# Performance work log

Measured on AMD Instinct MI355X. Metric: run time of the kernel, lower is better.

The kernel has to match this reference:

```python
import jax, jax.numpy as jnp
import numpy as np

B, N, D = 2, 4096, 256
H = 8
HD = D // H  # head dim = 32
DFF = 4 * D


def _layer_norm(x):
    # Matches source: (x - mean) / (std + 1e-6), std is population std (ddof=0)
    m = jnp.mean(x, axis=-1, keepdims=True)
    s = jnp.std(x, axis=-1, keepdims=True)
    return (x - m) / (s + 1e-6)


def setup_inputs() -> dict:
    key = jax.random.key(0)
    ks = jax.random.split(key, 11)
    sd = 1.0 / np.sqrt(D)
    sf = 1.0 / np.sqrt(DFF)
    return {
        "embeddings_in": jax.random.normal(ks[0], (B, N, D), dtype=jnp.float32),
        "Wq": jax.random.normal(ks[1], (D, D), dtype=jnp.float32) * sd,
        "bq": jnp.zeros((D,), dtype=jnp.float32),
        "Wk": jax.random.normal(ks[2], (D, D), dtype=jnp.float32) * sd,
        "bk": jnp.zeros((D,), dtype=jnp.float32),
        "Wv": jax.random.normal(ks[3], (D, D), dtype=jnp.float32) * sd,
        "bv": jnp.zeros((D,), dtype=jnp.float32),
        "Wo": jax.random.normal(ks[4], (D, D), dtype=jnp.float32) * sd,
        "bo": jnp.zeros((D,), dtype=jnp.float32),
        "W1": jax.random.normal(ks[5], (D, DFF), dtype=jnp.float32) * sd,
        "b1": jnp.zeros((DFF,), dtype=jnp.float32),
        "W2": jax.random.normal(ks[6], (DFF, D), dtype=jnp.float32) * sf,
        "b2": jnp.zeros((D,), dtype=jnp.float32),
    }


def reference(embeddings_in, Wq, bq, Wk, bk, Wv, bv, Wo, bo, W1, b1, W2, b2):
    x = embeddings_in
    xn1 = _layer_norm(x)
    # QKV projections, split into heads: [B,N,D] -> [B,H,N,HD]
    def heads(t):
        return jnp.transpose(t.reshape(B, N, H, HD), (0, 2, 1, 3))
    q = heads(xn1 @ Wq + bq)
    k = heads(xn1 @ Wk + bk)
    v = heads(xn1 @ Wv + bv)
    scores = jnp.einsum('bhnd,bhmd->bhnm', q, k) / jnp.sqrt(jnp.float32(HD))
    attn = jax.nn.softmax(scores, axis=-1)
    heads_out = jnp.einsum('bhnm,bhmd->bhnd', attn, v)
    attn_out = jnp.transpose(heads_out, (0, 2, 1, 3)).reshape(B, N, D)
    attn_out = attn_out @ Wo + bo  # dropout is identity in eval
    x_skip = attn_out + x
    xn2 = _layer_norm(x_skip)
    mlp = jax.nn.gelu(xn2 @ W1 + b1) @ W2 + b2
    return mlp + x_skip
```

## Files before the change

kernel.cpp:

```cpp
#include <hip/hip_runtime.h>
#include <hip/hip_bf16.h>

#define Bb 2
#define Nn 4096
#define Dd 256
#define Hh 8
#define HDh 32
#define DFFd 1024
#define MT (Bb*Nn)
#define Tt ((size_t)MT * Dd)
#define SPLIT 4
#define KVB (Nn / SPLIT)
#define NSTP (KVB / 64)

typedef __attribute__((ext_vector_type(8))) short short8;
typedef __attribute__((ext_vector_type(4))) float f32x4;
typedef __attribute__((address_space(1))) const unsigned int gu32;
typedef __attribute__((address_space(3))) unsigned int lu32;

__device__ __forceinline__ void gll16(const ushort* g, ushort* l) {
  __builtin_amdgcn_global_load_lds((gu32*)g, (lu32*)l, 16, 0, 0);
}
__device__ __forceinline__ float bf2f(ushort u){
  union { unsigned int i; float f; } v; v.i = ((unsigned int)u) << 16; return v.f;
}
__device__ __forceinline__ ushort f2bf(float f){
  union { float f; unsigned int i; } v; v.f = f;
  unsigned int r = v.i + 0x7fffu + ((v.i >> 16) & 1u);
  return (ushort)(r >> 16);
}
__device__ __forceinline__ int ars(int r){ return r * 64 + (r >> 3) * 32; }

__device__ __forceinline__ void ln_rows4(const float* __restrict__ x,
                                         ushort* __restrict__ out, int row0,
                                         int wave, int lane)
{
  #pragma unroll
  for (int r = 0; r < 4; r++) {
    const int row = row0 + wave * 4 + r;
    const float4 u = *(const float4*)(x + (size_t)row * Dd + lane * 4);
    float s1 = u.x + u.y + u.z + u.w;
    float s2 = u.x*u.x + u.y*u.y + u.z*u.z + u.w*u.w;
    #pragma unroll
    for (int m = 1; m < 64; m <<= 1) { s1 += __shfl_xor(s1, m, 64); s2 += __shfl_xor(s2, m, 64); }
    const float mean = s1 * (1.0f / Dd);
    float var = s2 * (1.0f / Dd) - mean * mean;
    var = var < 0.f ? 0.f : var;
    const float inv = 1.0f / (sqrtf(var) + 1e-6f);
    ushort4 o;
    o.x = f2bf((u.x - mean) * inv); o.y = f2bf((u.y - mean) * inv);
    o.z = f2bf((u.z - mean) * inv); o.w = f2bf((u.w - mean) * inv);
    *(ushort4*)(out + (size_t)row * Dd + lane * 4) = o;
  }
}

__global__ __launch_bounds__(256) void p0_kernel(
    const float* __restrict__ Wq, const float* __restrict__ Wk,
    const float* __restrict__ Wv, const float* __restrict__ Wo,
    const float* __restrict__ W1, const float* __restrict__ W2,
    const float* __restrict__ bq, const float* __restrict__ bk,
    const float* __restrict__ bv, ushort* __restrict__ wt,
    float* __restrict__ bqkv, const float* __restrict__ x,
    ushort* __restrict__ xn1)
{
  const int bid = blockIdx.x, t = threadIdx.x;
  __shared__ __align__(16) ushort T[64][72];
  if (bid < 192) {
    const float* src; ushort* dst; int Nsrc, Kdst, kt, nt;
    if (bid < 64) {
      const int m = bid >> 4, tile = bid & 15;
      kt = tile >> 2; nt = tile & 3; Nsrc = 256; Kdst = 256;
      src = (m == 0 ? Wq : m == 1 ? Wk : m == 2 ? Wv : Wo);
      dst = (m == 3) ? (wt + 196608) : (wt + m * 65536);
    } else if (bid < 128) {
      const int tile = bid - 64; kt = tile >> 4; nt = tile & 15;
      Nsrc = 1024; Kdst = 256; src = W1; dst = wt + 262144;
    } else {
      const int tile = bid - 128; kt = tile >> 2; nt = tile & 3;
      Nsrc = 256; Kdst = 1024; src = W2; dst = wt + 524288;
    }
    const int k0 = kt * 64, n0 = nt * 64;
    const int cc = t & 15, rr = t >> 4;
    #pragma unroll
    for (int pass = 0; pass < 4; pass++) {
      const int k = rr + pass * 16;
      const float4 v = *(const float4*)(src + (size_t)(k0 + k) * Nsrc + n0 + cc * 4);
      T[cc * 4 + 0][k] = f2bf(v.x); T[cc * 4 + 1][k] = f2bf(v.y);
      T[cc * 4 + 2][k] = f2bf(v.z); T[cc * 4 + 3][k] = f2bf(v.w);
    }
    __syncthreads();
    const int nl = t >> 2, ks = (t & 3) * 16;
    const short8 a = *(const short8*)(&T[nl][ks]);
    const short8 b = *(const short8*)(&T[nl][ks + 8]);
    ushort* drow = dst + (size_t)(n0 + nl) * Kdst + k0 + ks;
    *(short8*)(drow) = a; *(short8*)(drow + 8) = b;
  } else if (bid == 192) {
    bqkv[t] = bq[t]; bqkv[256 + t] = bk[t]; bqkv[512 + t] = bv[t];
  }
  ln_rows4(x, xn1, bid * 16, t >> 6, t & 63);
}

__global__ __launch_bounds__(256) void ln_kernel(const float* __restrict__ x,
                                                 ushort* __restrict__ out)
{
  ln_rows4(x, out, blockIdx.x * 16, threadIdx.x >> 6, threadIdx.x & 63);
}

template<int EPI>
__global__ __launch_bounds__(256) void gemm_wide(
    const ushort* __restrict__ A, const ushort* __restrict__ BT,
    const float* __restrict__ bias, void* __restrict__ outv, int N, int K)
{
  __shared__ __align__(16) ushort As[2][128 * 64];
  __shared__ __align__(16) ushort Bs[2][128 * 64];
  const int tid = threadIdx.x;
  const int wave = tid >> 6, lane = tid & 63;
  const int quad = lane >> 4, l15 = lane & 15;
  const int wm = wave >> 1, wn = wave & 1;
  const int n0 = blockIdx.x * 128, m0 = blockIdx.y * 128;
  f32x4 acc[4][4];
  #pragma unroll
  for (int mt = 0; mt < 4; mt++)
    #pragma unroll
    for (int nt = 0; nt < 4; nt++) acc[mt][nt] = (f32x4){0.f,0.f,0.f,0.f};
  const int srow = lane >> 3, scol = ((lane & 7) ^ srow) * 8;
  const ushort* gA[4];
  const ushort* gB[4];
  #pragma unroll
  for (int i = 0; i < 4; i++) {
    gA[i] = A  + (size_t)(m0 + i * 32 + wave * 8 + srow) * K + scol;
    gB[i] = BT + (size_t)(n0 + i * 32 + wave * 8 + srow) * K + scol;
  }
  int aoff[4], boff[4], cx[2];
  #pragma unroll
  for (int mt = 0; mt < 4; mt++) aoff[mt] = (wm * 64 + mt * 16 + l15) * 64;
  #pragma unroll
  for (int nt = 0; nt < 4; nt++) boff[nt] = (wn * 64 + nt * 16 + l15) * 64;
  #pragma unroll
  for (int kk = 0; kk < 2; kk++) cx[kk] = ((kk * 4 + quad) ^ (l15 & 7)) * 8;
  #pragma unroll
  for (int i = 0; i < 4; i++) {
    gll16(gA[i], &As[0][(i * 32 + wave * 8) * 64]);
    gll16(gB[i], &Bs[0][(i * 32 + wave * 8) * 64]);
  }
  __syncthreads();
  const int NC = K >> 6;
  int p = 0;
  for (int c = 0; c < NC; c++) {
    if (c + 1 < NC) {
      #pragma unroll
      for (int i = 0; i < 4; i++) {
        gll16(gA[i] + (c + 1) * 64, &As[p ^ 1][(i * 32 + wave * 8) * 64]);
        gll16(gB[i] + (c + 1) * 64, &Bs[p ^ 1][(i * 32 + wave * 8) * 64]);
      }
    }
    #pragma unroll
    for (int kk = 0; kk < 2; kk++) {
      short8 af[4];
      #pragma unroll
      for (int mt = 0; mt < 4; mt++)
        af[mt] = *(const short8*)(&As[p][aoff[mt] + cx[kk]]);
      #pragma unroll
      for (int nt = 0; nt < 4; nt++) {
        const short8 bf = *(const short8*)(&Bs[p][boff[nt] + cx[kk]]);
        #pragma unroll
        for (int mt = 0; mt < 4; mt++)
          acc[mt][nt] = __builtin_amdgcn_mfma_f32_16x16x32_bf16(af[mt], bf, acc[mt][nt], 0, 0, 0);
      }
    }
    __syncthreads();
    p ^= 1;
  }
  #pragma unroll
  for (int mt = 0; mt < 4; mt++) {
    const int row0 = m0 + wm * 64 + mt * 16 + quad * 4;
    #pragma unroll
    for (int nt = 0; nt < 4; nt++) {
      const int col = n0 + wn * 64 + nt * 16 + l15;
      const float bv = bias[col];
      float c[4];
      #pragma unroll
      for (int i = 0; i < 4; i++) c[i] = acc[mt][nt][i] + bv;
      if (EPI == 0) {
        ushort* qkv = (ushort*)outv;
        const int w = col >> 8, cd = col & 255;
        const int h = cd >> 5, hd = cd & 31;
        const int b = row0 >> 12, n = row0 & (Nn - 1);
        if (w < 2) {
          const float sc2 = (w == 0) ? (1.4426950408889634f * 0.17677669529663687f) : 1.0f;
          ushort* dst = qkv + (size_t)w * Tt + ((size_t)((b * Hh + h) * Nn) + n) * HDh + hd;
          #pragma unroll
          for (int i = 0; i < 4; i++) dst[(size_t)i * HDh] = f2bf(c[i] * sc2);
        } else {
          ushort4 pk;
          pk.x = f2bf(c[0]); pk.y = f2bf(c[1]); pk.z = f2bf(c[2]); pk.w = f2bf(c[3]);
          *(ushort4*)(qkv + 2 * Tt + ((size_t)((b * Hh + h) * HDh + hd)) * Nn + n) = pk;
        }
      } else {
        ushort* out = (ushort*)outv;
        #pragma unroll
        for (int i = 0; i < 4; i++) {
          const float t = tanhf(0.7978845608028654f * (c[i] + 0.044715f * c[i] * c[i] * c[i]));
          out[(size_t)(row0 + i) * N + col] = f2bf(0.5f * c[i] * (1.0f + t));
        }
      }
    }
  }
}

template<int EPI, int BM>
__global__ __launch_bounds__(256) void gemm_epi(
    const ushort* __restrict__ A, const ushort* __restrict__ BT,
    const float* __restrict__ bias, const float* __restrict__ res,
    void* __restrict__ outv, int N, int K)
{
  constexpr int MI = BM / 64;
  constexpr int AI = BM / 32;
  __shared__ __align__(16) ushort AsF[2][BM * 64 + (BM / 8) * 32];
  __shared__ __align__(16) ushort BsF[2][64 * 64 + 8 * 32];
  const int tid = threadIdx.x;
  const int wave = tid >> 6, lane = tid & 63;
  const int quad = lane >> 4, l15 = lane & 15;
  const int n0 = blockIdx.x * 64, m0 = blockIdx.y * BM;
  f32x4 acc[MI][4];
  #pragma unroll
  for (int mt = 0; mt < MI; mt++)
    #pragma unroll
    for (int nt = 0; nt < 4; nt++) acc[mt][nt] = (f32x4){0.f,0.f,0.f,0.f};
  const int srow = lane >> 3, scol = ((lane & 7) ^ srow) * 8;
  const ushort* gA[AI];
  #pragma unroll
  for (int ai = 0; ai < AI; ai++)
    gA[ai] = A + (size_t)(m0 + ai * 32 + wave * 8 + srow) * K + scol;
  const ushort* gB[2];
  #pragma unroll
  for (int bi = 0; bi < 2; bi++)
    gB[bi] = BT + (size_t)(n0 + bi * 32 + wave * 8 + srow) * K + scol;
  int aoff[MI], boff[4];
  #pragma unroll
  for (int mt = 0; mt < MI; mt++) aoff[mt] = ars(wave * 16 * MI + mt * 16 + l15);
  #pragma unroll
  for (int nt = 0; nt < 4; nt++) boff[nt] = ars(nt * 16 + l15);
  int cx[2];
  #pragma unroll
  for (int kk = 0; kk < 2; kk++) cx[kk] = ((kk * 4 + quad) ^ (l15 & 7)) * 8;
  #pragma unroll
  for (int ai = 0; ai < AI; ai++) gll16(gA[ai], &AsF[0][ars(ai * 32 + wave * 8)]);
  #pragma unroll
  for (int bi = 0; bi < 2; bi++) gll16(gB[bi], &BsF[0][ars(bi * 32 + wave * 8)]);
  __syncthreads();
  const int NC = K >> 6;
  int p = 0;
  for (int c = 0; c < NC; c++) {
    if (c + 1 < NC) {
      #pragma unroll
      for (int ai = 0; ai < AI; ai++)
        gll16(gA[ai] + (c + 1) * 64, &AsF[p ^ 1][ars(ai * 32 + wave * 8)]);
      #pragma unroll
      for (int bi = 0; bi < 2; bi++)
        gll16(gB[bi] + (c + 1) * 64, &BsF[p ^ 1][ars(bi * 32 + wave * 8)]);
    }
    #pragma unroll
    for (int kk = 0; kk < 2; kk++) {
      short8 af[MI];
      #pragma unroll
      for (int mt = 0; mt < MI; mt++)
        af[mt] = *(const short8*)(&AsF[p][aoff[mt] + cx[kk]]);
      #pragma unroll
      for (int nt = 0; nt < 4; nt++) {
        const short8 bf = *(const short8*)(&BsF[p][boff[nt] + cx[kk]]);
        #pragma unroll
        for (int mt = 0; mt < MI; mt++)
          acc[mt][nt] = __builtin_amdgcn_mfma_f32_16x16x32_bf16(af[mt], bf, acc[mt][nt], 0, 0, 0);
      }
    }
    __syncthreads();
    p ^= 1;
  }
  #pragma unroll
  for (int mt = 0; mt < MI; mt++) {
    const int row0 = m0 + wave * (16 * MI) + mt * 16 + quad * 4;
    #pragma unroll
    for (int nt = 0; nt < 4; nt++) {
      const int col = n0 + nt * 16 + l15;
      const float bv = bias[col];
      float c[4];
      #pragma unroll
      for (int i = 0; i < 4; i++) c[i] = acc[mt][nt][i] + bv;
      if (EPI == 1) {
        float* out = (float*)outv;
        #pragma unroll
        for (int i = 0; i < 4; i++) {
          const size_t idx = (size_t)(row0 + i) * N + col;
          out[idx] = c[i] + res[idx];
        }
      } else {
        ushort* out = (ushort*)outv;
        #pragma unroll
        for (int i = 0; i < 4; i++) {
          const float t = tanhf(0.7978845608028654f * (c[i] + 0.044715f * c[i] * c[i] * c[i]));
          out[(size_t)(row0 + i) * N + col] = f2bf(0.5f * c[i] * (1.0f + t));
        }
      }
    }
  }
}

__global__ __launch_bounds__(256, 4) void attn_kernel(
    const ushort* __restrict__ qp, const ushort* __restrict__ kp,
    const ushort* __restrict__ vtg, ushort* __restrict__ op0,
    ushort* __restrict__ op123, float* __restrict__ lp)
{
  __shared__ __align__(16) ushort Ks[2][64][32];
  __shared__ __align__(16) ushort Vt[2][32][72];
  __shared__ __align__(16) ushort Ps[4][64][40];
  const int tid = threadIdx.x;
  const int wave = tid >> 6, lane = tid & 63;
  const int quad = lane >> 4, l15 = lane & 15;
  const int qtb = blockIdx.x, bh = blockIdx.y, sp = blockIdx.z;
  const size_t base = (size_t)bh * Nn * HDh;
  const int q0 = qtb * 256 + wave * 64;
  short8 qf[4];
  #pragma unroll
  for (int qt = 0; qt < 4; qt++)
    qf[qt] = *(const short8*)(qp + base + (size_t)(q0 + qt * 16 + l15) * HDh + quad * 8);
  const int kv0 = sp * KVB;
  const ushort* kg = kp + base + (size_t)(kv0 + wave * 16 + (lane >> 2)) * HDh
                   + (((lane & 3) ^ ((lane >> 3) & 3)) * 8);
  const int kc = (quad ^ ((l15 >> 1) & 3)) * 8;
  const int vr = tid >> 3, vc = (tid & 7) * 8;
  const ushort* vg = vtg + base + (size_t)vr * Nn + kv0 + vc;
  ushort* psw = &Ps[wave][0][0];
  f32x4 o[2][4], ol[4];
  #pragma unroll
  for (int qt = 0; qt < 4; qt++) {
    o[0][qt] = (f32x4){0,0,0,0}; o[1][qt] = (f32x4){0,0,0,0};
    ol[qt] = (f32x4){0,0,0,0};
  }
  const short one = (short)0x3F80;
  const short8 ones = {one,one,one,one,one,one,one,one};
  const f32x4 zero4 = {0,0,0,0};
  const float SA = 8388608.0f;
  const float SB = 1065102389.0f;
  gll16(kg, &Ks[0][wave * 16][0]);
  int4 vreg = *(const int4*)vg;
  *(int4*)(&Vt[0][vr][vc]) = vreg;
  vreg = *(const int4*)(vg + 64);
  __syncthreads();
  #pragma unroll 2
  for (int step = 0; step < NSTP; step++) {
    const int p = step & 1;
    if (step + 1 < NSTP) {
      gll16(kg + (size_t)(step + 1) * 64 * HDh, &Ks[p ^ 1][wave * 16][0]);
      *(int4*)(&Vt[p ^ 1][vr][vc]) = vreg;
    }
    if (step + 2 < NSTP) vreg = *(const int4*)(vg + (size_t)(step + 2) * 64);
    #pragma unroll
    for (int half = 0; half < 2; half++) {
      #pragma unroll
      for (int nt2 = 0; nt2 < 2; nt2++) {
        const int nt = half * 2 + nt2;
        const short8 kf = *(const short8*)(&Ks[p][nt * 16 + l15][kc]);
        #pragma unroll
        for (int qt = 0; qt < 4; qt++) {
          const f32x4 s = __builtin_amdgcn_mfma_f32_16x16x32_bf16(kf, qf[qt], zero4, 0, 0, 0);
          const unsigned int i0 = (unsigned int)(int)fmaf(s[0], SA, SB);
          const unsigned int i1 = (unsigned int)(int)fmaf(s[1], SA, SB);
          const unsigned int i2 = (unsigned int)(int)fmaf(s[2], SA, SB);
          const unsigned int i3 = (unsigned int)(int)fmaf(s[3], SA, SB);
          uint2 pk;
          pk.x = __builtin_amdgcn_perm(i1, i0, 0x07060302u);
          pk.y = __builtin_amdgcn_perm(i3, i2, 0x07060302u);
          *(uint2*)(psw + (qt * 16 + l15) * 40 + nt2 * 16 + quad * 4) = pk;
        }
      }
      __builtin_amdgcn_wave_barrier();
      const short8 v0 = *(const short8*)(&Vt[p][l15][half * 32 + quad * 8]);
      const short8 v1 = *(const short8*)(&Vt[p][16 + l15][half * 32 + quad * 8]);
      #pragma unroll
      for (int qt = 0; qt < 4; qt++) {
        const short8 pb = *(const short8*)(psw + (qt * 16 + l15) * 40 + quad * 8);
        o[0][qt] = __builtin_amdgcn_mfma_f32_16x16x32_bf16(v0, pb, o[0][qt], 0, 0, 0);
        o[1][qt] = __builtin_amdgcn_mfma_f32_16x16x32_bf16(v1, pb, o[1][qt], 0, 0, 0);
        ol[qt]   = __builtin_amdgcn_mfma_f32_16x16x32_bf16(ones, pb, ol[qt], 0, 0, 0);
      }
      __builtin_amdgcn_wave_barrier();
    }
    __syncthreads();
  }
  lp[(size_t)sp * (16 * Nn) + (size_t)bh * Nn + q0 + lane] = ol[lane >> 4][0];
  ushort* ob = (sp == 0 ? op0 : op123 + (size_t)(sp - 1) * (16 * (size_t)Nn * HDh));
  #pragma unroll
  for (int pass = 0; pass < 2; pass++) {
    #pragma unroll
    for (int qt2 = 0; qt2 < 2; qt2++) {
      const int qt = pass * 2 + qt2;
      #pragma unroll
      for (int dt = 0; dt < 2; dt++) {
        ushort4 pk;
        pk.x = f2bf(o[dt][qt][0]); pk.y = f2bf(o[dt][qt][1]);
        pk.z = f2bf(o[dt][qt][2]); pk.w = f2bf(o[dt][qt][3]);
        *(ushort4*)(psw + (qt2 * 16 + l15) * 40 + dt * 16 + quad * 4) = pk;
      }
    }
    __builtin_amdgcn_wave_barrier();
    #pragma unroll
    for (int j = 0; j < 2; j++) {
      const int row = j * 16 + (lane >> 2);
      const short8 ov = *(const short8*)(psw + row * 40 + (lane & 3) * 8);
      const int q = q0 + pass * 32 + row;
      *(short8*)(ob + ((size_t)bh * Nn + q) * HDh + (lane & 3) * 8) = ov;
    }
    __builtin_amdgcn_wave_barrier();
  }
}

__global__ __launch_bounds__(256) void attn_combine(
    const ushort* __restrict__ op0, const ushort* __restrict__ op123,
    const float* __restrict__ lp, ushort* __restrict__ attn)
{
  const int idx = blockIdx.x * 256 + threadIdx.x;
  const int d8 = idx & 3, n = (idx >> 2) & (Nn - 1), bh = idx >> 14;
  const size_t ln = (size_t)bh * Nn + n;
  float l = 0.f;
  #pragma unroll
  for (int sp = 0; sp < SPLIT; sp++) l += lp[(size_t)sp * (16 * Nn) + ln];
  const float inv = 1.0f / l;
  float acc[8];
  #pragma unroll
  for (int k = 0; k < 8; k++) acc[k] = 0.f;
  const size_t qoff = ln * HDh + d8 * 8;
  #pragma unroll
  for (int sp = 0; sp < SPLIT; sp++) {
    const ushort* src = (sp == 0 ? op0 : op123 + (size_t)(sp - 1) * (16 * (size_t)Nn * HDh)) + qoff;
    const short8 u = *(const short8*)src;
    #pragma unroll
    for (int k = 0; k < 8; k++) acc[k] += bf2f((ushort)u[k]);
  }
  short8 ov;
  #pragma unroll
  for (int k = 0; k < 8; k++) ov[k] = (short)f2bf(acc[k] * inv);
  const int b = bh >> 3, h = bh & 7;
  *(short8*)(attn + ((size_t)(b * Nn + n)) * Dd + h * HDh + d8 * 8) = ov;
}

extern "C" void kernel_launch(void* const* d_in, const int* in_sizes, int n_in,
                              void* d_out, int out_size, void* d_ws, size_t ws_size,
                              hipStream_t stream)
{
  const float* x  = (const float*)d_in[0];
  const float* Wq = (const float*)d_in[1];
  const float* bq = (const float*)d_in[2];
  const float* Wk = (const float*)d_in[3];
  const float* bk = (const float*)d_in[4];
  const float* Wv = (const float*)d_in[5];
  const float* bv = (const float*)d_in[6];
  const float* Wo = (const float*)d_in[7];
  const float* bo = (const float*)d_in[8];
  const float* W1 = (const float*)d_in[9];
  const float* b1 = (const float*)d_in[10];
  const float* W2 = (const float*)d_in[11];
  const float* b2 = (const float*)d_in[12];

  char* ws = (char*)d_ws;
  ushort* wt    = (ushort*)ws;
  ushort* wtqkv = wt;
  ushort* wto   = wt + 196608;
  ushort* wt1   = wt + 262144;
  ushort* wt2   = wt + 524288;
  float*  bqkv  = (float*)(ws + 786432 * 2);
  ushort* s0    = (ushort*)(ws + 786432 * 2 + 4096);
  ushort* s1    = s0 + Tt;
  ushort* s2    = s1 + Tt;
  ushort* s3    = s2 + Tt;
  float*  xsk   = (float*)(s3 + Tt);
  ushort* xn2   = (ushort*)(xsk + Tt);
  ushort* xn1   = s0;
  ushort* hid   = s0;
  ushort* op0   = s0;
  ushort* op123 = (ushort*)xsk;
  float*  lp    = (float*)d_out;
  ushort* attnb = (ushort*)((char*)d_out + (4u << 20));
  float*  outp  = (float*)d_out;

  const dim3 blk(256);
  hipLaunchKernelGGL(p0_kernel, dim3(512), blk, 0, stream,
                     Wq, Wk, Wv, Wo, W1, W2, bq, bk, bv, wt, bqkv, x, xn1);
  hipLaunchKernelGGL((gemm_wide<0>), dim3(6, 64), blk, 0, stream,
                     xn1, wtqkv, bqkv, (void*)s1, 768, Dd);

  hipLaunchKernelGGL(attn_kernel, dim3(Nn / 256, Bb * Hh, SPLIT), blk, 0, stream,
                     s1, s2, s3, op0, op123, lp);
  hipLaunchKernelGGL(attn_combine, dim3((Bb * Hh * Nn * 4) / 256), blk, 0, stream,
                     op0, op123, lp, attnb);

  hipLaunchKernelGGL((gemm_epi<1,64>), dim3(4, 128), blk, 0, stream,
                     attnb, wto, bo, x, (void*)xsk, Dd, Dd);
  hipLaunchKernelGGL(ln_kernel, dim3(MT / 16), blk, 0, stream, xsk, xn2);
  hipLaunchKernelGGL((gemm_wide<2>), dim3(8, 64), blk, 0, stream,
                     xn2, wt1, b1, (void*)hid, DFFd, Dd);
  hipLaunchKernelGGL((gemm_epi<1,64>), dim3(4, 128), blk, 0, stream,
                     hid, wt2, b2, xsk, (void*)outp, Dd, DFFd);
}
```

Measured before the change: 193.2 us.

## Fuse MLP up-projection, GELU and down-projection into one kernel

Replaces the two MLP GEMM launches with a single kernel. Each block handles 32 rows, computes 256-wide chunks of the hidden layer with GELU into shared memory, and accumulates the down-projection straight away. This avoids writing the 8192x1024 bf16 hidden tensor to global memory and reading it back, and drops one launch. In exchange there are only 256 blocks with large LDS use, so occupancy and parallelism drop, and both weight matrices are streamed again by every block.

```diff
diff --git a/kernel.cpp b/kernel.cpp
--- a/kernel.cpp
+++ b/kernel.cpp
@@ -203,6 +203,132 @@
           const float t = tanhf(0.7978845608028654f * (c[i] + 0.044715f * c[i] * c[i] * c[i]));
           out[(size_t)(row0 + i) * N + col] = f2bf(0.5f * c[i] * (1.0f + t));
         }
+      }
+    }
+  }
+}
+
+__global__ __launch_bounds__(256) void gemm_mlp(
+    const ushort* __restrict__ A, const ushort* __restrict__ B1T,
+    const float* __restrict__ b1, const ushort* __restrict__ B2T,
+    const float* __restrict__ b2, const float* __restrict__ res,
+    float* __restrict__ out)
+{
+  __shared__ __align__(16) ushort As[128 * 64];
+  __shared__ __align__(16) ushort Bs[2][256 * 64];
+  __shared__ __align__(16) ushort Hs[32][264];
+  const int tid = threadIdx.x;
+  const int wave = tid >> 6, lane = tid & 63;
+  const int quad = lane >> 4, l15 = lane & 15;
+  const int m0 = blockIdx.x * 32;
+  const int srow = lane >> 3, scol = ((lane & 7) ^ srow) * 8;
+  int cx[2];
+  #pragma unroll
+  for (int kk = 0; kk < 2; kk++) cx[kk] = ((kk * 4 + quad) ^ (l15 & 7)) * 8;
+  #pragma unroll
+  for (int i = 0; i < 4; i++)
+    gll16(A + (size_t)(m0 + i * 8 + srow) * 256 + wave * 64 + scol,
+          &As[(wave * 32 + i * 8) * 64]);
+  #pragma unroll
+  for (int i = 0; i < 8; i++)
+    gll16(B1T + (size_t)(wave * 64 + i * 8 + srow) * 256 + scol,
+          &Bs[0][(wave * 64 + i * 8) * 64]);
+  __syncthreads();
+  f32x4 acc2[2][4];
+  #pragma unroll
+  for (int mt = 0; mt < 2; mt++)
+    #pragma unroll
+    for (int nt = 0; nt < 4; nt++) acc2[mt][nt] = (f32x4){0.f,0.f,0.f,0.f};
+  int p = 0;
+  for (int j = 0; j < 4; j++) {
+    f32x4 acc1[2][4];
+    #pragma unroll
+    for (int mt = 0; mt < 2; mt++)
+      #pragma unroll
+      for (int nt = 0; nt < 4; nt++) acc1[mt][nt] = (f32x4){0.f,0.f,0.f,0.f};
+    #pragma unroll
+    for (int s = 0; s < 4; s++) {
+      if (s < 3) {
+        #pragma unroll
+        for (int i = 0; i < 8; i++)
+          gll16(B1T + (size_t)(j * 256 + wave * 64 + i * 8 + srow) * 256 + (s + 1) * 64 + scol,
+                &Bs[p ^ 1][(wave * 64 + i * 8) * 64]);
+      } else {
+        #pragma unroll
+        for (int i = 0; i < 8; i++)
+          gll16(B2T + (size_t)(wave * 64 + i * 8 + srow) * 1024 + j * 256 + scol,
+                &Bs[p ^ 1][(wave * 64 + i * 8) * 64]);
+      }
+      #pragma unroll
+      for (int kk = 0; kk < 2; kk++) {
+        short8 af[2];
+        #pragma unroll
+        for (int mt = 0; mt < 2; mt++)
+          af[mt] = *(const short8*)(&As[(s * 32 + mt * 16 + l15) * 64 + cx[kk]]);
+        #pragma unroll
+        for (int nt = 0; nt < 4; nt++) {
+          const short8 bf = *(const short8*)(&Bs[p][(wave * 64 + nt * 16 + l15) * 64 + cx[kk]]);
+          #pragma unroll
+          for (int mt = 0; mt < 2; mt++)
+            acc1[mt][nt] = __builtin_amdgcn_mfma_f32_16x16x32_bf16(af[mt], bf, acc1[mt][nt], 0, 0, 0);
+        }
+      }
+      __syncthreads(); p ^= 1;
+    }
+    #pragma unroll
+    for (int nt = 0; nt < 4; nt++) {
+      const float bv = b1[j * 256 + wave * 64 + nt * 16 + l15];
+      #pragma unroll
+      for (int mt = 0; mt < 2; mt++)
+        #pragma unroll
+        for (int i = 0; i < 4; i++) {
+          const float c = acc1[mt][nt][i] + bv;
+          const float t = tanhf(0.7978845608028654f * (c + 0.044715f * c * c * c));
+          Hs[mt * 16 + quad * 4 + i][wave * 64 + nt * 16 + l15] = f2bf(0.5f * c * (1.0f + t));
+        }
+    }
+    __syncthreads();
+    #pragma unroll
+    for (int s = 0; s < 4; s++) {
+      if (s < 3) {
+        #pragma unroll
+        for (int i = 0; i < 8; i++)
+          gll16(B2T + (size_t)(wave * 64 + i * 8 + srow) * 1024 + j * 256 + (s + 1) * 64 + scol,
+                &Bs[p ^ 1][(wave * 64 + i * 8) * 64]);
+      } else if (j < 3) {
+        #pragma unroll
+        for (int i = 0; i < 8; i++)
+          gll16(B1T + (size_t)((j + 1) * 256 + wave * 64 + i * 8 + srow) * 256 + scol,
+                &Bs[p ^ 1][(wave * 64 + i * 8) * 64]);
+      }
+      #pragma unroll
+      for (int kk = 0; kk < 2; kk++) {
+        short8 af[2];
+        #pragma unroll
+        for (int mt = 0; mt < 2; mt++)
+          af[mt] = *(const short8*)(&Hs[mt * 16 + l15][s * 64 + kk * 32 + quad * 8]);
+        #pragma unroll
+        for (int nt = 0; nt < 4; nt++) {
+          const short8 bf = *(const short8*)(&Bs[p][(wave * 64 + nt * 16 + l15) * 64 + cx[kk]]);
+          #pragma unroll
+          for (int mt = 0; mt < 2; mt++)
+            acc2[mt][nt] = __builtin_amdgcn_mfma_f32_16x16x32_bf16(af[mt], bf, acc2[mt][nt], 0, 0, 0);
+        }
+      }
+      __syncthreads(); p ^= 1;
+    }
+  }
+  #pragma unroll
+  for (int mt = 0; mt < 2; mt++) {
+    const int row0 = m0 + mt * 16 + quad * 4;
+    #pragma unroll
+    for (int nt = 0; nt < 4; nt++) {
+      const int col = wave * 64 + nt * 16 + l15;
+      const float bv = b2[col];
+      #pragma unroll
+      for (int i = 0; i < 4; i++) {
+        const size_t idx = (size_t)(row0 + i) * Dd + col;
+        out[idx] = acc2[mt][nt][i] + bv + res[idx];
       }
     }
   }
@@ -476,7 +602,6 @@
   float*  xsk   = (float*)(s3 + Tt);
   ushort* xn2   = (ushort*)(xsk + Tt);
   ushort* xn1   = s0;
-  ushort* hid   = s0;
   ushort* op0   = s0;
   ushort* op123 = (ushort*)xsk;
   float*  lp    = (float*)d_out;
@@ -497,8 +622,6 @@
   hipLaunchKernelGGL((gemm_epi<1,64>), dim3(4, 128), blk, 0, stream,
                      attnb, wto, bo, x, (void*)xsk, Dd, Dd);
   hipLaunchKernelGGL(ln_kernel, dim3(MT / 16), blk, 0, stream, xsk, xn2);
-  hipLaunchKernelGGL((gemm_wide<2>), dim3(8, 64), blk, 0, stream,
-                     xn2, wt1, b1, (void*)hid, DFFd, Dd);
-  hipLaunchKernelGGL((gemm_epi<1,64>), dim3(4, 128), blk, 0, stream,
-                     hid, wt2, b2, xsk, (void*)outp, Dd, DFFd);
-}
+  hipLaunchKernelGGL(gemm_mlp, dim3(MT / 32), blk, 0, stream,
+                     xn2, wt1, b1, wt2, b2, xsk, outp);
+}
```

After: 202.5 us. +4.8%, slower.
